# Optimization experiments

Hardware: AMD Instinct MI355X
Metric: run time of the kernel (lower is better)

## Reference

```python
import jax, jax.numpy as jnp
import numpy as np

DEPTH = 6
HEADS = 4
DH = 64
MAXLEN = 512

def layer_norm(x, s, b, eps=1e-5):
    m = jnp.mean(x, axis=-1, keepdims=True)
    v = jnp.var(x, axis=-1, keepdims=True)
    return (x - m) / jnp.sqrt(v + eps) * s + b

def setup_inputs() -> dict:
    key = jax.random.key(0)
    ks = jax.random.split(key, 8)
    D = 256
    inner = HEADS * DH  # 256
    hid = 1024          # int(256 * 4.0)
    init = lambda k, shape: jax.random.normal(k, shape, jnp.float32) * 0.02
    return {
        "x": jax.random.normal(ks[0], (8, 12, 512, 256), jnp.float32),
        "ln1_s": jnp.ones((DEPTH, D), jnp.float32), "ln1_b": jnp.zeros((DEPTH, D), jnp.float32),
        "qkv_w": init(ks[1], (DEPTH, D, 3 * inner)), "qkv_b": jnp.zeros((DEPTH, 3 * inner), jnp.float32),
        "proj_w": init(ks[2], (DEPTH, inner, D)), "proj_b": jnp.zeros((DEPTH, D), jnp.float32),
        "rel_table": init(ks[3], (DEPTH, 2 * MAXLEN - 1, HEADS)),
        "ln2_s": jnp.ones((DEPTH, D), jnp.float32), "ln2_b": jnp.zeros((DEPTH, D), jnp.float32),
        "w1": init(ks[4], (DEPTH, D, hid)), "b1": jnp.zeros((DEPTH, hid), jnp.float32),
        "w2": init(ks[5], (DEPTH, hid, D)), "b2": jnp.zeros((DEPTH, D), jnp.float32),
        "lnf_s": jnp.ones((D,), jnp.float32), "lnf_b": jnp.zeros((D,), jnp.float32),
    }

def reference(x, ln1_s, ln1_b, qkv_w, qkv_b, proj_w, proj_b, rel_table,
              ln2_s, ln2_b, w1, b1, w2, b2, lnf_s, lnf_b):
    B, L, N, D = x.shape
    h = x.reshape(B * L, N, D)  # (b l) n d
    idx = jnp.arange(N)
    rel_idx = idx[:, None] - idx[None, :] + MAXLEN - 1  # (N, N) in [0, 2*MAXLEN-2]
    scale = DH ** -0.5
    for d in range(DEPTH):
        # pre-norm attention with relative position bias
        xn = layer_norm(h, ln1_s[d], ln1_b[d])
        qkv = xn @ qkv_w[d] + qkv_b[d]
        q, k, v = jnp.split(qkv, 3, axis=-1)
        split_heads = lambda t: t.reshape(B * L, N, HEADS, DH).transpose(0, 2, 1, 3)
        q, k, v = split_heads(q), split_heads(k), split_heads(v)
        bias = rel_table[d][rel_idx].transpose(2, 0, 1)  # (H, N, N)
        scores = jnp.einsum('bhid,bhjd->bhij', q, k) * scale + bias[None]
        attn = jax.nn.softmax(scores, axis=-1)
        o = jnp.einsum('bhij,bhjd->bhid', attn, v)
        o = o.transpose(0, 2, 1, 3).reshape(B * L, N, HEADS * DH)
        h = h + (o @ proj_w[d] + proj_b[d])
        # pre-norm FFN
        xn2 = layer_norm(h, ln2_s[d], ln2_b[d])
        h = h + (jax.nn.gelu(xn2 @ w1[d] + b1[d]) @ w2[d] + b2[d])
    h = layer_norm(h, lnf_s, lnf_b)
    return h.reshape(B, L, N, D)
```

## Files before the change

kernel.cpp:

```cpp
#include <hip/hip_runtime.h>
#include <math.h>

#define T_TOK 49152
#define DMODEL 256
#define NSEQ 512
#define BLROWS 96
#define LOG2E 1.4426950408889634f

typedef unsigned short ushortT;
using frag_ab = __attribute__((ext_vector_type(8))) short;
using f32x4   = __attribute__((ext_vector_type(4))) float;

__device__ __forceinline__ ushortT f2b(float f) {
    union { float f; unsigned int u; } v; v.f = f;
    unsigned int u = v.u;
    u += 0x7FFFu + ((u >> 16) & 1u);
    return (ushortT)(u >> 16);
}
__device__ __forceinline__ float b2f(ushortT h) {
    union { unsigned int u; float f; } v; v.u = ((unsigned int)h) << 16;
    return v.f;
}

#if __has_builtin(__builtin_amdgcn_exp2f)
#define FEXP2(x) __builtin_amdgcn_exp2f(x)
#else
#define FEXP2(x) __expf((x) * 0.6931471805599453f)
#endif

__device__ __forceinline__ unsigned int cvtpk_bf16(float lo, float hi) {
    unsigned int r;
    asm("v_cvt_pk_bf16_f32 %0, %1, %2" : "=v"(r) : "v"(lo), "v"(hi));
    return r;
}

__device__ __forceinline__ void gload_lds16(const ushortT* g, ushortT* l) {
    __builtin_amdgcn_global_load_lds(
        (const __attribute__((address_space(1))) unsigned int*)g,
        (__attribute__((address_space(3))) unsigned int*)l, 16, 0, 0);
}

__global__ __launch_bounds__(256) void wprep_kernel(const float* __restrict__ qkv_w,
                                                    const float* __restrict__ proj_w,
                                                    const float* __restrict__ w1,
                                                    const float* __restrict__ w2,
                                                    ushortT* __restrict__ out) {
    __shared__ float Ls[64][132];
    int bid = blockIdx.x;
    int d = bid / 96, t = bid % 96;
    const float* src; int N, KS; size_t dbase; int tt;
    if (t < 24)      { src = qkv_w  + (size_t)d * 256 * 768;  N = 768;  KS = 4;  dbase = (size_t)d * 196608;            tt = t;      }
    else if (t < 32) { src = proj_w + (size_t)d * 256 * 256;  N = 256;  KS = 4;  dbase = 1179648 + (size_t)d * 65536;   tt = t - 24; }
    else if (t < 64) { src = w1     + (size_t)d * 256 * 1024; N = 1024; KS = 4;  dbase = 1572864 + (size_t)d * 262144;  tt = t - 32; }
    else             { src = w2     + (size_t)d * 1024 * 256; N = 256;  KS = 16; dbase = 3145728 + (size_t)d * 262144;  tt = t - 64; }
    int nb = tt / KS, ks = tt % KS;
    int k0 = ks * 64, n0 = nb * 128;
    int tid = threadIdx.x;
#pragma unroll
    for (int i = 0; i < 8; ++i) {
        int fidx = tid + i * 256;
        int kk = fidx >> 5, ng = fidx & 31;
        float4 v = *(const float4*)(src + (size_t)(k0 + kk) * N + n0 + ng * 4);
        *(float4*)&Ls[kk][ng * 4] = v;
    }
    __syncthreads();
    int n = tid & 127, kh = tid >> 7;
    ushortT* dst = out + dbase + (size_t)tt * 8192 + n * 64 + kh * 32;
    ushortT tmp[32];
#pragma unroll
    for (int j = 0; j < 32; ++j) tmp[j] = f2b(Ls[kh * 32 + j][n]);
#pragma unroll
    for (int u = 0; u < 4; ++u) *(uint4*)(dst + u * 8) = *(uint4*)(tmp + u * 8);
}

template <bool OB>
__global__ __launch_bounds__(256) void ln_kernel(const float* __restrict__ in,
                                                 void* __restrict__ out,
                                                 const float* __restrict__ s,
                                                 const float* __restrict__ b) {
    int wave = threadIdx.x >> 6;
    int lane = threadIdx.x & 63;
    size_t row = (size_t)blockIdx.x * 4 + wave;
    float4 v = reinterpret_cast<const float4*>(in + row * DMODEL)[lane];
    float sum = v.x + v.y + v.z + v.w;
    float ssq = v.x * v.x + v.y * v.y + v.z * v.z + v.w * v.w;
#pragma unroll
    for (int m = 1; m <= 32; m <<= 1) {
        sum += __shfl_xor(sum, m, 64);
        ssq += __shfl_xor(ssq, m, 64);
    }
    float mean = sum * (1.0f / 256.0f);
    float var = ssq * (1.0f / 256.0f) - mean * mean;
    float rstd = rsqrtf(var + 1e-5f);
    float4 sv = reinterpret_cast<const float4*>(s)[lane];
    float4 bv = reinterpret_cast<const float4*>(b)[lane];
    float o0 = (v.x - mean) * rstd * sv.x + bv.x;
    float o1 = (v.y - mean) * rstd * sv.y + bv.y;
    float o2 = (v.z - mean) * rstd * sv.z + bv.z;
    float o3 = (v.w - mean) * rstd * sv.w + bv.w;
    if (OB) {
        ushortT* po = (ushortT*)out + row * DMODEL + lane * 4;
        ushort4 ov; ov.x = f2b(o0); ov.y = f2b(o1); ov.z = f2b(o2); ov.w = f2b(o3);
        *(ushort4*)po = ov;
    } else {
        float4 ov; ov.x = o0; ov.y = o1; ov.z = o2; ov.w = o3;
        reinterpret_cast<float4*>((float*)out + row * DMODEL)[lane] = ov;
    }
}

template <int EPI>
__global__ __launch_bounds__(256) void gemm_bf16(const ushortT* __restrict__ A,
                                                 const ushortT* __restrict__ Wt,
                                                 const float* __restrict__ bias,
                                                 float* __restrict__ R,
                                                 ushortT* __restrict__ Cb,
                                                 int K, int N) {
    __shared__ ushortT smem[32768];
    const int nb = blockIdx.x, n0 = nb * 128;
    const int m0 = blockIdx.y * 128;
    const int tid = threadIdx.x, lane = tid & 63, wave = tid >> 6;
    const int wr = wave >> 1, wc = wave & 1;
    const int KS = K >> 6;
    const size_t wtile = (size_t)nb * KS * 8192;

    const int rA = lane >> 3;
    const int colsw = (lane & 7) ^ rA;

    auto STAGE = [&](int buf, int kt) {
        ushortT* Ad = smem + buf * 16384;
        ushortT* Bd = Ad + 8192;
#pragma unroll
        for (int c2 = 0; c2 < 4; ++c2) {
            int rb = wave * 32 + c2 * 8;
            int row = rb + rA;
            gload_lds16(A + (size_t)(m0 + row) * K + kt * 64 + colsw * 8,
                        Ad + rb * 64);
            gload_lds16(Wt + wtile + (size_t)kt * 8192 + row * 64 + colsw * 8,
                        Bd + rb * 64);
        }
    };

    f32x4 acc[4][4];
#pragma unroll
    for (int i = 0; i < 4; ++i)
#pragma unroll
        for (int j = 0; j < 4; ++j) acc[i][j] = (f32x4)0.0f;

    STAGE(0, 0);
    __syncthreads();
    int cur = 0;
    for (int kt = 0; kt < KS; ++kt) {
        if (kt + 1 < KS) STAGE(cur ^ 1, kt + 1);
        const ushortT* Ab = smem + cur * 16384;
        const ushortT* Bb = Ab + 8192;
#pragma unroll
        for (int kst = 0; kst < 2; ++kst) {
            frag_ab af[4], bf4[4];
            int ku = kst * 4 + (lane >> 4);
#pragma unroll
            for (int f = 0; f < 4; ++f) {
                int row = wr * 64 + f * 16 + (lane & 15);
                af[f] = *(const frag_ab*)&Ab[row * 64 + ((ku ^ (row & 7)) << 3)];
                int col = wc * 64 + f * 16 + (lane & 15);
                bf4[f] = *(const frag_ab*)&Bb[col * 64 + ((ku ^ (col & 7)) << 3)];
            }
#pragma unroll
            for (int mf = 0; mf < 4; ++mf)
#pragma unroll
                for (int nf = 0; nf < 4; ++nf)
                    acc[mf][nf] = __builtin_amdgcn_mfma_f32_16x16x32_bf16(
                        af[mf], bf4[nf], acc[mf][nf], 0, 0, 0);
        }
        __syncthreads();
        cur ^= 1;
    }

    const int cg = lane >> 4, cl = lane & 15;
    if (EPI != 2) {
        ushortT* Cs = smem;
#pragma unroll
        for (int nf = 0; nf < 4; ++nf) {
            int col = wc * 64 + nf * 16 + cl;
            float bv = bias[n0 + col];
#pragma unroll
            for (int mf = 0; mf < 4; ++mf)
#pragma unroll
                for (int r = 0; r < 4; ++r) {
                    int row = wr * 64 + mf * 16 + cg * 4 + r;
                    float c = acc[mf][nf][r] + bv;
                    if (EPI == 1) {
                        c = c / (1.0f + __expf(-1.5957691216f * (c + 0.044715f * c * c * c)));
                    }
                    Cs[row * 128 + (((col >> 3) ^ (row & 7)) << 3) + (col & 7)] = f2b(c);
                }
        }
        __syncthreads();
#pragma unroll
        for (int it = 0; it < 8; ++it) {
            int idx = tid + it * 256;
            int row = idx >> 4, u = idx & 15;
            uint4 v = *(uint4*)&Cs[row * 128 + ((u ^ (row & 7)) << 3)];
            *(uint4*)&Cb[(size_t)(m0 + row) * N + n0 + u * 8] = v;
        }
    } else {
        float* Cf = (float*)smem;
#pragma unroll
        for (int h = 0; h < 2; ++h) {
            if (wr == h) {
#pragma unroll
                for (int nf = 0; nf < 4; ++nf) {
                    int col = wc * 64 + nf * 16 + cl;
                    float bv = bias[n0 + col];
#pragma unroll
                    for (int mf = 0; mf < 4; ++mf)
#pragma unroll
                        for (int r = 0; r < 4; ++r) {
                            int rl = mf * 16 + cg * 4 + r;
                            Cf[rl * 128 + (((col >> 2) ^ (rl & 7)) << 2) + (col & 3)] =
                                acc[mf][nf][r] + bv;
                        }
                }
            }
            __syncthreads();
#pragma unroll
            for (int it = 0; it < 8; ++it) {
                int idx = tid + it * 256;
                int row2 = idx >> 5, u = idx & 31;
                float4 c4 = *(float4*)&Cf[row2 * 128 + ((u ^ (row2 & 7)) << 2)];
                float* rp = R + (size_t)(m0 + h * 64 + row2) * N + n0 + u * 4;
                float4 r4 = *(float4*)rp;
                r4.x += c4.x; r4.y += c4.y; r4.z += c4.z; r4.w += c4.w;
                *(float4*)rp = r4;
            }
            if (h == 0) __syncthreads();
        }
    }
}

__global__ __launch_bounds__(512) void attn_kernel(const ushortT* __restrict__ qkv,
                                                   const float* __restrict__ rel,
                                                   ushortT* __restrict__ o) {
    __shared__ ushortT Ks[2][64 * 64];
    __shared__ ushortT Vt[2][64 * 72];
    __shared__ ushortT Ps[128 * 64];
    __shared__ float   rl[1024];

    const int pair = blockIdx.x, qb = blockIdx.y;
    const int bl = pair >> 2, hh = pair & 3;
    const int tid = threadIdx.x;
    const int lane = tid & 63, w = tid >> 6;
    const int c15 = lane & 15, g = lane >> 4;
    const size_t base = (size_t)bl * NSEQ * 768;
    const int qoff = hh * 64, koff = 256 + hh * 64, voff = 512 + hh * 64;
    const int i0 = qb * 128;

    for (int i = tid; i < 1023; i += 512) rl[i] = rel[(size_t)i * 4 + hh] * LOG2E;

    const int sj = tid >> 3, sdg = tid & 7;
    const ushortT* kvb = qkv + base;
    auto KSTAGE = [&](int buf, int kt) {
        gload_lds16(kvb + (size_t)(kt * 64 + sj) * 768 + koff + ((sdg ^ (sj & 7)) << 3),
                    &Ks[buf][0] + (size_t)w * 512);
    };
    uint4 vreg;
    auto VLOAD = [&](int kt) {
        vreg = *(const uint4*)(kvb + (size_t)(kt * 64 + sj) * 768 + voff + sdg * 8);
    };
    auto VWRITE = [&](int buf) {
        ushortT tmp[8];
        *(uint4*)tmp = vreg;
        int jc = sj ^ (sdg << 3);
#pragma unroll
        for (int e = 0; e < 8; ++e) Vt[buf][(sdg * 8 + e) * 72 + jc] = tmp[e];
    };

    frag_ab qf[2];
    {
        const ushortT* qp = kvb + (size_t)(i0 + w * 16 + c15) * 768 + qoff + g * 8;
        qf[0] = *(const frag_ab*)(qp);
        qf[1] = *(const frag_ab*)(qp + 32);
    }

    float m_i[4], l_i[4];
    f32x4 oacc[4];
#pragma unroll
    for (int r = 0; r < 4; ++r) { m_i[r] = -1e30f; l_i[r] = 0.0f; }
#pragma unroll
    for (int nf = 0; nf < 4; ++nf) oacc[nf] = (f32x4)0.0f;

    const int irow = w * 16 + g * 4;

    VLOAD(0);
    KSTAGE(0, 0);
    VWRITE(0);
    __syncthreads();

    int cur = 0;
    for (int kt = 0; kt < 8; ++kt) {
        if (kt < 7) { KSTAGE(cur ^ 1, kt + 1); VLOAD(kt + 1); }

        f32x4 sacc[4];
#pragma unroll
        for (int nf = 0; nf < 4; ++nf) sacc[nf] = (f32x4)0.0f;
        __builtin_amdgcn_s_setprio(1);
#pragma unroll
        for (int kst = 0; kst < 2; ++kst) {
            int ku = kst * 4 + g;
#pragma unroll
            for (int nf = 0; nf < 4; ++nf) {
                int j = nf * 16 + c15;
                frag_ab kf = *(frag_ab*)&Ks[cur][j * 64 + ((ku ^ (j & 7)) << 3)];
                sacc[nf] = __builtin_amdgcn_mfma_f32_16x16x32_bf16(qf[kst], kf, sacc[nf], 0, 0, 0);
            }
        }
        __builtin_amdgcn_s_setprio(0);

        float sv[4][4];
        const int rlb = i0 + irow - kt * 64 - c15 + 511;
#pragma unroll
        for (int nf = 0; nf < 4; ++nf)
#pragma unroll
            for (int r = 0; r < 4; ++r)
                sv[nf][r] = sacc[nf][r] * (0.125f * LOG2E) + rl[rlb + r - nf * 16];

        float rmax[4];
#pragma unroll
        for (int r = 0; r < 4; ++r) {
            float rm = fmaxf(fmaxf(sv[0][r], sv[1][r]), fmaxf(sv[2][r], sv[3][r]));
#pragma unroll
            for (int m = 1; m <= 8; m <<= 1) rm = fmaxf(rm, __shfl_xor(rm, m, 64));
            rmax[r] = rm;
        }
        bool cskip = true;
#pragma unroll
        for (int r = 0; r < 4; ++r) cskip = cskip && (rmax[r] <= m_i[r] + 11.5f);
        if (!__all(cskip)) {
#pragma unroll
            for (int r = 0; r < 4; ++r) {
                float mn = fmaxf(m_i[r], rmax[r]);
                float cr = FEXP2(m_i[r] - mn);
                m_i[r] = mn;
                l_i[r] *= cr;
#pragma unroll
                for (int nf = 0; nf < 4; ++nf) oacc[nf][r] *= cr;
            }
        }

        float psum[4] = {0.0f, 0.0f, 0.0f, 0.0f};
        unsigned int words[4][4];
#pragma unroll
        for (int nf = 0; nf < 4; ++nf)
#pragma unroll
            for (int r = 0; r < 4; ++r) {
                float p = FEXP2(sv[nf][r] - m_i[r]);
                psum[r] += p;
                float po = __shfl_xor(p, 1, 64);
                words[nf][r] = cvtpk_bf16(p, po);
            }
#pragma unroll
        for (int r = 0; r < 4; ++r) {
#pragma unroll
            for (int m = 1; m <= 8; m <<= 1) psum[r] += __shfl_xor(psum[r], m, 64);
            l_i[r] += psum[r];
        }

        if (kt < 7) VWRITE(cur ^ 1);

        if (!(lane & 1)) {
#pragma unroll
            for (int nf = 0; nf < 4; ++nf) {
                int j2 = nf * 16 + c15;
#pragma unroll
                for (int r = 0; r < 4; ++r) {
                    int i = irow + r;
                    *(unsigned int*)&Ps[i * 64 + ((((j2 >> 3) ^ (i & 7))) << 3) + (j2 & 7)] =
                        words[nf][r];
                }
            }
        }

        __builtin_amdgcn_s_setprio(1);
#pragma unroll
        for (int ks2 = 0; ks2 < 2; ++ks2) {
            int ip = w * 16 + c15;
            int jb = ks2 * 32 + g * 8;
            frag_ab pf = *(frag_ab*)&Ps[ip * 64 + (((jb >> 3) ^ (ip & 7)) << 3)];
#pragma unroll
            for (int nf = 0; nf < 4; ++nf) {
                int dh = nf * 16 + c15;
                int jv = jb ^ ((dh >> 3) << 3);
                frag_ab vf = *(frag_ab*)&Vt[cur][dh * 72 + jv];
                oacc[nf] = __builtin_amdgcn_mfma_f32_16x16x32_bf16(pf, vf, oacc[nf], 0, 0, 0);
            }
        }
        __builtin_amdgcn_s_setprio(0);

        __syncthreads();
        cur ^= 1;
    }

    float inv[4];
#pragma unroll
    for (int r = 0; r < 4; ++r) inv[r] = 1.0f / l_i[r];
#pragma unroll
    for (int nf = 0; nf < 4; ++nf)
#pragma unroll
        for (int r = 0; r < 4; ++r) {
            float own = oacc[nf][r] * inv[r];
            float other = __shfl_xor(own, 1, 64);
            if (!(lane & 1)) {
                size_t trow = (size_t)bl * NSEQ + i0 + irow + r;
                *(unsigned int*)&o[trow * DMODEL + hh * 64 + nf * 16 + c15] =
                    cvtpk_bf16(own, other);
            }
        }
}

extern "C" void kernel_launch(void* const* d_in, const int* in_sizes, int n_in,
                              void* d_out, int out_size, void* d_ws, size_t ws_size,
                              hipStream_t stream) {
    const float* x       = (const float*)d_in[0];
    const float* ln1_s   = (const float*)d_in[1];
    const float* ln1_b   = (const float*)d_in[2];
    const float* qkv_w   = (const float*)d_in[3];
    const float* qkv_b   = (const float*)d_in[4];
    const float* proj_w  = (const float*)d_in[5];
    const float* proj_b  = (const float*)d_in[6];
    const float* rel_tab = (const float*)d_in[7];
    const float* ln2_s   = (const float*)d_in[8];
    const float* ln2_b   = (const float*)d_in[9];
    const float* w1      = (const float*)d_in[10];
    const float* b1      = (const float*)d_in[11];
    const float* w2      = (const float*)d_in[12];
    const float* b2      = (const float*)d_in[13];
    const float* lnf_s   = (const float*)d_in[14];
    const float* lnf_b   = (const float*)d_in[15];

    float* h = (float*)d_out;
    ushortT* wsu = (ushortT*)d_ws;
    const size_t WPRE = 4718592;

    static const int cands[12] = {1, 2, 3, 4, 6, 8, 12, 16, 24, 32, 48, 96};
    int NC = 96;
    for (int i = 0; i < 12; ++i) {
        size_t tc = (size_t)T_TOK / cands[i];
        if (WPRE * 2 + tc * 3072 <= ws_size) { NC = cands[i]; break; }
    }
    const int TC = T_TOK / NC;
    const int BLC = BLROWS / NC;
    ushortT* xnC = wsu + WPRE;
    ushortT* big = xnC + (size_t)TC * 256;
    ushortT* oC  = big + (size_t)TC * 1024;

    wprep_kernel<<<576, 256, 0, stream>>>(qkv_w, proj_w, w1, w2, wsu);
    hipMemcpyAsync(h, x, (size_t)T_TOK * DMODEL * sizeof(float),
                   hipMemcpyDeviceToDevice, stream);

    dim3 blk(256);
    for (int d = 0; d < 6; ++d) {
        for (int c = 0; c < NC; ++c) {
            float* hc = h + (size_t)c * TC * DMODEL;
            ln_kernel<true><<<TC / 4, blk, 0, stream>>>(hc, xnC, ln1_s + d * 256, ln1_b + d * 256);
            gemm_bf16<0><<<dim3(6, TC / 128), blk, 0, stream>>>(
                xnC, wsu + (size_t)d * 196608, qkv_b + d * 768, nullptr, big, 256, 768);
            attn_kernel<<<dim3(BLC * 4, NSEQ / 128), 512, 0, stream>>>(
                big, rel_tab + (size_t)d * 1023 * 4, oC);
            gemm_bf16<2><<<dim3(2, TC / 128), blk, 0, stream>>>(
                oC, wsu + 1179648 + (size_t)d * 65536, proj_b + d * 256, hc, nullptr, 256, 256);
        }
        for (int c = 0; c < NC; ++c) {
            float* hc = h + (size_t)c * TC * DMODEL;
            ln_kernel<true><<<TC / 4, blk, 0, stream>>>(hc, xnC, ln2_s + d * 256, ln2_b + d * 256);
            gemm_bf16<1><<<dim3(8, TC / 128), blk, 0, stream>>>(
                xnC, wsu + 1572864 + (size_t)d * 262144, b1 + d * 1024, nullptr, big, 256, 1024);
            gemm_bf16<2><<<dim3(2, TC / 128), blk, 0, stream>>>(
                big, wsu + 3145728 + (size_t)d * 262144, b2 + d * 256, hc, nullptr, 1024, 256);
        }
    }
    ln_kernel<false><<<T_TOK / 4, blk, 0, stream>>>(h, h, lnf_s, lnf_b);
}
```

Before: 2.081 ms.

## Compute softmax row sums via MFMA with ones and use DPP row max

Replaces the shuffle-based row-max reduction with DPP row_shr ops inside 16-lane rows, and removes the butterfly shuffle reduction of the softmax denominator by accumulating row sums through an extra MFMA of the P tile against a vector of bf16 ones. P values are now written to LDS as individual 16-bit stores per lane instead of packed pairs via a shuffle. This cuts cross-lane shuffle traffic in the attention inner loop. In exchange it adds MFMA work and doubles the number of narrower LDS stores, and the denominator is summed from bf16-rounded P, which may change numerics slightly.

```diff
diff --git a/kernel.cpp b/kernel.cpp
--- a/kernel.cpp
+++ b/kernel.cpp
@@ -32,6 +32,20 @@
     unsigned int r;
     asm("v_cvt_pk_bf16_f32 %0, %1, %2" : "=v"(r) : "v"(lo), "v"(hi));
     return r;
+}
+
+__device__ __forceinline__ float rowmax16(float x) {
+    union { float f; int i; } u, v;
+    u.f = x;
+    v.i = __builtin_amdgcn_update_dpp(0, u.i, 0x121, 0xf, 0xf, true);
+    x = fmaxf(x, v.f); u.f = x;
+    v.i = __builtin_amdgcn_update_dpp(0, u.i, 0x122, 0xf, 0xf, true);
+    x = fmaxf(x, v.f); u.f = x;
+    v.i = __builtin_amdgcn_update_dpp(0, u.i, 0x124, 0xf, 0xf, true);
+    x = fmaxf(x, v.f); u.f = x;
+    v.i = __builtin_amdgcn_update_dpp(0, u.i, 0x128, 0xf, 0xf, true);
+    x = fmaxf(x, v.f);
+    return x;
 }
 
 __device__ __forceinline__ void gload_lds16(const ushortT* g, ushortT* l) {
@@ -281,12 +295,17 @@
         qf[1] = *(const frag_ab*)(qp + 32);
     }
 
-    float m_i[4], l_i[4];
-    f32x4 oacc[4];
-#pragma unroll
-    for (int r = 0; r < 4; ++r) { m_i[r] = -1e30f; l_i[r] = 0.0f; }
+    frag_ab ones1;
+#pragma unroll
+    for (int e = 0; e < 8; ++e) ones1[e] = (short)0x3F80;
+
+    float m_i[4];
+    f32x4 oacc[4], lacc;
+#pragma unroll
+    for (int r = 0; r < 4; ++r) m_i[r] = -1e30f;
 #pragma unroll
     for (int nf = 0; nf < 4; ++nf) oacc[nf] = (f32x4)0.0f;
+    lacc = (f32x4)0.0f;
 
     const int irow = w * 16 + g * 4;
 
@@ -325,12 +344,9 @@
 
         float rmax[4];
 #pragma unroll
-        for (int r = 0; r < 4; ++r) {
-            float rm = fmaxf(fmaxf(sv[0][r], sv[1][r]), fmaxf(sv[2][r], sv[3][r]));
-#pragma unroll
-            for (int m = 1; m <= 8; m <<= 1) rm = fmaxf(rm, __shfl_xor(rm, m, 64));
-            rmax[r] = rm;
-        }
+        for (int r = 0; r < 4; ++r)
+            rmax[r] = rowmax16(fmaxf(fmaxf(sv[0][r], sv[1][r]), fmaxf(sv[2][r], sv[3][r])));
+
         bool cskip = true;
 #pragma unroll
         for (int r = 0; r < 4; ++r) cskip = cskip && (rmax[r] <= m_i[r] + 11.5f);
@@ -340,44 +356,25 @@
                 float mn = fmaxf(m_i[r], rmax[r]);
                 float cr = FEXP2(m_i[r] - mn);
                 m_i[r] = mn;
-                l_i[r] *= cr;
+                lacc[r] *= cr;
 #pragma unroll
                 for (int nf = 0; nf < 4; ++nf) oacc[nf][r] *= cr;
             }
         }
 
-        float psum[4] = {0.0f, 0.0f, 0.0f, 0.0f};
-        unsigned int words[4][4];
-#pragma unroll
-        for (int nf = 0; nf < 4; ++nf)
+#pragma unroll
+        for (int nf = 0; nf < 4; ++nf) {
+            int j2 = nf * 16 + c15;
 #pragma unroll
             for (int r = 0; r < 4; ++r) {
                 float p = FEXP2(sv[nf][r] - m_i[r]);
-                psum[r] += p;
-                float po = __shfl_xor(p, 1, 64);
-                words[nf][r] = cvtpk_bf16(p, po);
-            }
-#pragma unroll
-        for (int r = 0; r < 4; ++r) {
-#pragma unroll
-            for (int m = 1; m <= 8; m <<= 1) psum[r] += __shfl_xor(psum[r], m, 64);
-            l_i[r] += psum[r];
+                unsigned int pw = cvtpk_bf16(p, p);
+                int i = irow + r;
+                Ps[i * 64 + (((j2 >> 3) ^ (i & 7)) << 3) + (j2 & 7)] = (ushortT)pw;
+            }
         }
 
         if (kt < 7) VWRITE(cur ^ 1);
-
-        if (!(lane & 1)) {
-#pragma unroll
-            for (int nf = 0; nf < 4; ++nf) {
-                int j2 = nf * 16 + c15;
-#pragma unroll
-                for (int r = 0; r < 4; ++r) {
-                    int i = irow + r;
-                    *(unsigned int*)&Ps[i * 64 + ((((j2 >> 3) ^ (i & 7))) << 3) + (j2 & 7)] =
-                        words[nf][r];
-                }
-            }
-        }
 
         __builtin_amdgcn_s_setprio(1);
 #pragma unroll
@@ -385,6 +382,7 @@
             int ip = w * 16 + c15;
             int jb = ks2 * 32 + g * 8;
             frag_ab pf = *(frag_ab*)&Ps[ip * 64 + (((jb >> 3) ^ (ip & 7)) << 3)];
+            lacc = __builtin_amdgcn_mfma_f32_16x16x32_bf16(pf, ones1, lacc, 0, 0, 0);
 #pragma unroll
             for (int nf = 0; nf < 4; ++nf) {
                 int dh = nf * 16 + c15;
@@ -401,7 +399,7 @@
 
     float inv[4];
 #pragma unroll
-    for (int r = 0; r < 4; ++r) inv[r] = 1.0f / l_i[r];
+    for (int r = 0; r < 4; ++r) inv[r] = 1.0f / lacc[r];
 #pragma unroll
     for (int nf = 0; nf < 4; ++nf)
 #pragma unroll
```

Result: faster. 1.846 ms (-11.3%).
